# Performance work log

Measured on AMD Instinct MI355X. Metric: run time of the kernel, lower is better.

The kernel has to match this reference:

```python
import jax, jax.numpy as jnp
import numpy as np

QP = 127.0          # signed symmetric 8-bit: Qp = 2**(8-1)-1
MIN_RANGE = 1e-6


def _ste_round(q):
    # round_pass: straight-through estimator round
    return q + jax.lax.stop_gradient(jnp.round(q) - q)


def _quant_per_token(x):
    # symmetric per-token: amax over last dim, keepdim
    s = jnp.clip(jnp.max(jnp.abs(x), axis=-1, keepdims=True), MIN_RANGE, None) / QP
    return _ste_round(x / s), s


def _quant_per_tensor(w):
    s = jnp.clip(jnp.max(jnp.abs(w)), MIN_RANGE, None) / QP
    return _ste_round(w / s), s


def _qlinear(x2d, w, b):
    # fake-quant linear: quantize act per-token, weight per-tensor,
    # int-domain matmul, bias added before dequant rescale (faithful to source)
    qx, sx = _quant_per_token(x2d)      # [N,K], [N,1]
    qw, sw = _quant_per_tensor(w)       # [M,K], scalar
    out = jnp.matmul(qx, qw.T) + b[None, :]
    return out * (sx * sw)              # [N,M]


def setup_inputs() -> dict:
    key = jax.random.key(0)
    k1, k2, k3, k4, k5 = jax.random.split(key, 5)
    B, S, D, H = 64, 197, 768, 3072
    return {
        "x": jax.random.normal(k1, (B, S, D), dtype=jnp.float32),
        "w1": jax.random.normal(k2, (H, D), dtype=jnp.float32) * 0.02,
        "b1": jax.random.normal(k3, (H,), dtype=jnp.float32) * 0.02,
        "w2": jax.random.normal(k4, (D, H), dtype=jnp.float32) * 0.02,
        "b2": jax.random.normal(k5, (D,), dtype=jnp.float32) * 0.02,
    }


def reference(x, w1, b1, w2, b2):
    B, S, D = x.shape
    x2d = x.reshape(-1, D)                         # view(-1, x.size(-1))
    h = _qlinear(x2d, w1, b1)                      # fc1
    h = jax.nn.gelu(h, approximate=False)          # ViT Mlp activation (exact GELU)
    o = _qlinear(h, w2, b2)                        # fc2
    return o.reshape(B, S, -1)
```

## Files before the change

### kernel.cpp

```cpp
#include <hip/hip_runtime.h>
#include <stdint.h>

#define QPF  127.0f
#define MINR 1e-6f

typedef int v4i __attribute__((ext_vector_type(4)));
typedef float f4v __attribute__((ext_vector_type(4)));
typedef _Float16 h4v __attribute__((ext_vector_type(4)));
typedef _Float16 h8 __attribute__((ext_vector_type(8)));
typedef signed char c8 __attribute__((ext_vector_type(8)));

__device__ __forceinline__ float wave_max64(float v) {
  v = fmaxf(v, __shfl_xor(v, 32, 64));
  v = fmaxf(v, __shfl_xor(v, 16, 64));
  v = fmaxf(v, __shfl_xor(v, 8, 64));
  v = fmaxf(v, __shfl_xor(v, 4, 64));
  v = fmaxf(v, __shfl_xor(v, 2, 64));
  v = fmaxf(v, __shfl_xor(v, 1, 64));
  return v;
}

__device__ __forceinline__ float gelu_exact(float x) {
  float z = fabsf(x) * 0.70710678118654752440f;
  float t = __builtin_amdgcn_rcpf(fmaf(0.3275911f, z, 1.0f));
  float p = fmaf(fmaf(fmaf(fmaf(1.061405429f, t, -1.453152027f), t,
                           1.421413741f), t, -0.284496736f), t, 0.254829592f) * t;
  float e = __expf(-z * z);
  float erfz = fmaf(-p, e, 1.0f);
  float cdf = fmaf(0.5f, copysignf(erfz, x), 0.5f);
  return x * cdf;
}

__device__ __forceinline__ void gl2lds16(const void* g, void* l) {
  __builtin_amdgcn_global_load_lds(
      (const __attribute__((address_space(1))) int*)g,
      (__attribute__((address_space(3))) int*)l,
      16, 0, 0);
}

__global__ __launch_bounds__(256) void pre_kernel(
    const float* __restrict__ w1, const float* __restrict__ w2, int n4,
    const float* __restrict__ x, signed char* __restrict__ qx,
    float* __restrict__ sx, unsigned* __restrict__ amaxh,
    float* __restrict__ partial, int K, int nTok) {
  __shared__ float red[4];
  const int b = blockIdx.x;
  const int tid = threadIdx.x;
  const int lane = tid & 63, wvi = tid >> 6;

  if (b < 1024) {
    const float4* w4 = (const float4*)(b < 512 ? w1 : w2);
    const int bb = b & 511;
    float m = 0.f;
    for (int i = bb * 256 + tid; i < n4; i += 512 * 256) {
      float4 v = w4[i];
      m = fmaxf(m, fmaxf(fmaxf(fabsf(v.x), fabsf(v.y)),
                         fmaxf(fabsf(v.z), fabsf(v.w))));
    }
    m = wave_max64(m);
    if (lane == 0) red[wvi] = m;
    __syncthreads();
    if (tid == 0)
      partial[b] = fmaxf(fmaxf(red[0], red[1]), fmaxf(red[2], red[3]));
  } else {
    const int token = b - 1024;
    const float4* xr = (const float4*)(x + (size_t)token * K);
    const int k4 = K >> 2;
    float m = 0.f;
    float4 v = {0.f, 0.f, 0.f, 0.f};
    if (tid < k4) {
      v = xr[tid];
      m = fmaxf(fmaxf(fabsf(v.x), fabsf(v.y)), fmaxf(fabsf(v.z), fabsf(v.w)));
    }
    m = wave_max64(m);
    if (lane == 0) red[wvi] = m;
    __syncthreads();
    const float M = fmaxf(fmaxf(red[0], red[1]), fmaxf(red[2], red[3]));
    const float s = fmaxf(M, MINR) / QPF;
    const float rs = 1.0f / s;
    if (tid == 0) { sx[token] = s; amaxh[token] = 0u; }
    if (tid < k4) {
      char4 c;
      c.x = (signed char)(int)rintf(v.x * rs);
      c.y = (signed char)(int)rintf(v.y * rs);
      c.z = (signed char)(int)rintf(v.z * rs);
      c.w = (signed char)(int)rintf(v.w * rs);
      ((char4*)(qx + (size_t)token * K))[tid] = c;
    }
  }
}

__global__ __launch_bounds__(256) void wquant2_kernel(
    const float* __restrict__ w1, const float* __restrict__ w2, int n4,
    const float* __restrict__ partial, unsigned* __restrict__ wamax,
    signed char* __restrict__ q1, signed char* __restrict__ q2) {
  __shared__ float red[4];
  const int tid = threadIdx.x;
  const int lane = tid & 63, wvi = tid >> 6;
  const int y = blockIdx.y;
  float m = fmaxf(partial[y * 512 + tid], partial[y * 512 + 256 + tid]);
  m = wave_max64(m);
  if (lane == 0) red[wvi] = m;
  __syncthreads();
  const float M = fmaxf(fmaxf(red[0], red[1]), fmaxf(red[2], red[3]));
  if (blockIdx.x == 0 && tid == 0) wamax[y] = __float_as_uint(M);
  const float s = fmaxf(M, MINR) / QPF;
  const float rs = 1.0f / s;
  const float4* w4 = (const float4*)(y ? w2 : w1);
  char4* q4 = (char4*)(y ? q2 : q1);
  for (int i = blockIdx.x * 256 + tid; i < n4; i += gridDim.x * 256) {
    float4 v = w4[i];
    char4 c;
    c.x = (signed char)(int)rintf(v.x * rs);
    c.y = (signed char)(int)rintf(v.y * rs);
    c.z = (signed char)(int)rintf(v.z * rs);
    c.w = (signed char)(int)rintf(v.w * rs);
    q4[i] = c;
  }
}

__global__ __launch_bounds__(256) void hquant4_kernel(
    const _Float16* __restrict__ h, const unsigned* __restrict__ amaxbits,
    signed char* __restrict__ qh, float* __restrict__ sh, int K) {
  const int token = blockIdx.x * 4 + (threadIdx.x >> 6);
  const int lane = threadIdx.x & 63;
  const float s = fmaxf(__uint_as_float(amaxbits[token]), MINR) / QPF;
  const float rs = 1.0f / s;
  if (lane == 0) sh[token] = s;
  const h8* hr = (const h8*)(h + (size_t)token * K);
  c8* qr = (c8*)(qh + (size_t)token * K);
  for (int i = lane; i < (K >> 3); i += 64) {
    h8 v = hr[i];
    c8 c;
#pragma unroll
    for (int j = 0; j < 8; j++)
      c[j] = (signed char)(int)rintf((float)v[j] * rs);
    qr[i] = c;
  }
}

__global__ __launch_bounds__(256, 2) void gemm1_i8(
    const signed char* __restrict__ A, const signed char* __restrict__ B,
    const float* __restrict__ bias, const float* __restrict__ sA,
    const unsigned* __restrict__ sBbits, _Float16* __restrict__ out,
    unsigned* __restrict__ amax_out, int N, int K, int Mout) {
  __shared__ __align__(16) signed char lds[3 * 16384];

  const int t = threadIdx.x;
  const int lane = t & 63;
  const int wv = t >> 6;
  const int wm = wv >> 1;
  const int wn = wv & 1;
  const int rowBlk = blockIdx.y * 128;
  const int colBlk = blockIdx.x * 128;

  int ar0 = rowBlk + wv * 16 + (lane >> 2);
  int ar1 = ar0 + 64;
  if (ar0 > N - 1) ar0 = N - 1;
  if (ar1 > N - 1) ar1 = N - 1;
  const int br0 = colBlk + wv * 16 + (lane >> 2);
  const int br1 = br0 + 64;
  const int kb = (((lane & 3) ^ ((lane >> 3) & 3)) * 16);

  const signed char* gA0 = A + (size_t)ar0 * K + kb;
  const signed char* gA1 = A + (size_t)ar1 * K + kb;
  const signed char* gB0 = B + (size_t)br0 * K + kb;
  const signed char* gB1 = B + (size_t)br1 * K + kb;

  const v4i vzero = {0, 0, 0, 0};
  v4i acc[4][4];
#pragma unroll
  for (int i = 0; i < 4; i++)
#pragma unroll
    for (int j = 0; j < 4; j++) acc[i][j] = vzero;

  const int swz = ((lane >> 4) ^ ((lane >> 1) & 3)) * 16;
  const int aoff = (wm * 64 + (lane & 15)) * 64 + swz;
  const int boff = (wn * 64 + (lane & 15)) * 64 + swz + 8192;

  const int T = K >> 6;

  auto issue = [&](int bufo) {
    signed char* a = lds + bufo + wv * 1024;
    gl2lds16(gA0, a);
    gl2lds16(gA1, a + 4096);
    gl2lds16(gB0, a + 8192);
    gl2lds16(gB1, a + 12288);
    gA0 += 64; gA1 += 64; gB0 += 64; gB1 += 64;
  };

  issue(0);
  issue(16384);

  int cur = 0;
  for (int kt = 0; kt < T; ++kt) {
    asm volatile("" ::: "memory");
    if (kt < T - 1)
      __builtin_amdgcn_s_waitcnt(0x0074);
    else
      __builtin_amdgcn_s_waitcnt(0x0070);
    __builtin_amdgcn_s_barrier();
    asm volatile("" ::: "memory");

    if (kt + 2 < T) {
      int pf = cur + 32768;
      if (pf >= 49152) pf -= 49152;
      issue(pf);
    }

    v4i a[4], b[4];
#pragma unroll
    for (int mi = 0; mi < 4; mi++)
      a[mi] = *(const v4i*)(lds + cur + aoff + mi * 1024);
#pragma unroll
    for (int ni = 0; ni < 4; ni++)
      b[ni] = *(const v4i*)(lds + cur + boff + ni * 1024);
#pragma unroll
    for (int mi = 0; mi < 4; mi++)
#pragma unroll
      for (int ni = 0; ni < 4; ni++)
        acc[mi][ni] = __builtin_amdgcn_mfma_i32_16x16x64_i8(b[ni], a[mi],
                                                            acc[mi][ni], 0, 0, 0);
    cur += 16384;
    if (cur >= 49152) cur = 0;
  }

  const float sB = fmaxf(__uint_as_float(*sBbits), MINR) / QPF;
  const int col0 = colBlk + wn * 64 + (lane >> 4) * 4;

  f4v bv[4];
#pragma unroll
  for (int ni = 0; ni < 4; ni++) bv[ni] = *(const f4v*)(bias + col0 + ni * 16);

#pragma unroll
  for (int mi = 0; mi < 4; mi++) {
    const int grow = rowBlk + wm * 64 + mi * 16 + (lane & 15);
    const float ss = ((grow < N) ? sA[grow] : 0.f) * sB;
    float rmax = 0.f;
#pragma unroll
    for (int ni = 0; ni < 4; ni++) {
      h4v hv;
#pragma unroll
      for (int r = 0; r < 4; r++) {
        float v = ((float)acc[mi][ni][r] + bv[ni][r]) * ss;
        v = gelu_exact(v);
        rmax = fmaxf(rmax, fabsf(v));
        hv[r] = (_Float16)v;
      }
      if (grow < N)
        *(h4v*)(out + (size_t)grow * Mout + col0 + ni * 16) = hv;
    }
    rmax = fmaxf(rmax, __shfl_xor(rmax, 16, 64));
    rmax = fmaxf(rmax, __shfl_xor(rmax, 32, 64));
    if (lane < 16 && grow < N)
      atomicMax(amax_out + grow, __float_as_uint(rmax));
  }
}

__global__ __launch_bounds__(128, 2) void gemm2_i8(
    const signed char* __restrict__ A, const signed char* __restrict__ B,
    const float* __restrict__ bias, const float* __restrict__ sA,
    const unsigned* __restrict__ sBbits, float* __restrict__ out,
    int N, int K, int Mout) {
  __shared__ __align__(16) signed char lds[3 * 12288];

  const int t = threadIdx.x;
  const int lane = t & 63;
  const int wv = t >> 6;
  const int rowBlk = blockIdx.y * 128;
  const int colBlk = blockIdx.x * 64;

  const int trow = t >> 2;
  const int kb = (((t & 3) ^ ((t >> 3) & 3)) * 16);

  int ar[4];
#pragma unroll
  for (int i = 0; i < 4; i++) {
    ar[i] = rowBlk + i * 32 + trow;
    if (ar[i] > N - 1) ar[i] = N - 1;
  }
  const signed char* gA0 = A + (size_t)ar[0] * K + kb;
  const signed char* gA1 = A + (size_t)ar[1] * K + kb;
  const signed char* gA2 = A + (size_t)ar[2] * K + kb;
  const signed char* gA3 = A + (size_t)ar[3] * K + kb;
  const signed char* gB0 = B + (size_t)(colBlk + trow) * K + kb;
  const signed char* gB1 = B + (size_t)(colBlk + 32 + trow) * K + kb;

  const v4i vzero = {0, 0, 0, 0};
  v4i acc[4][4];
#pragma unroll
  for (int i = 0; i < 4; i++)
#pragma unroll
    for (int j = 0; j < 4; j++) acc[i][j] = vzero;

  const int swz = ((lane >> 4) ^ ((lane >> 1) & 3)) * 16;
  const int aoff = (wv * 64 + (lane & 15)) * 64 + swz;
  const int boff = 8192 + (lane & 15) * 64 + swz;

  const int T = K >> 6;

  auto issue = [&](int bufo) {
    signed char* p = lds + bufo + t * 16;
    gl2lds16(gA0, p);
    gl2lds16(gA1, p + 2048);
    gl2lds16(gA2, p + 4096);
    gl2lds16(gA3, p + 6144);
    gl2lds16(gB0, p + 8192);
    gl2lds16(gB1, p + 10240);
    gA0 += 64; gA1 += 64; gA2 += 64; gA3 += 64; gB0 += 64; gB1 += 64;
  };

  issue(0);
  issue(12288);

  int cur = 0;
  for (int kt = 0; kt < T; ++kt) {
    asm volatile("" ::: "memory");
    if (kt < T - 1)
      __builtin_amdgcn_s_waitcnt(0x0076);
    else
      __builtin_amdgcn_s_waitcnt(0x0070);
    __builtin_amdgcn_s_barrier();
    asm volatile("" ::: "memory");

    if (kt + 2 < T) {
      int pf = cur + 24576;
      if (pf >= 36864) pf -= 36864;
      issue(pf);
    }

    v4i a[4], b[4];
#pragma unroll
    for (int mi = 0; mi < 4; mi++)
      a[mi] = *(const v4i*)(lds + cur + aoff + mi * 1024);
#pragma unroll
    for (int ni = 0; ni < 4; ni++)
      b[ni] = *(const v4i*)(lds + cur + boff + ni * 1024);
#pragma unroll
    for (int mi = 0; mi < 4; mi++)
#pragma unroll
      for (int ni = 0; ni < 4; ni++)
        acc[mi][ni] = __builtin_amdgcn_mfma_i32_16x16x64_i8(b[ni], a[mi],
                                                            acc[mi][ni], 0, 0, 0);
    cur += 12288;
    if (cur >= 36864) cur = 0;
  }

  const float sB = fmaxf(__uint_as_float(*sBbits), MINR) / QPF;
  const int col0 = colBlk + (lane >> 4) * 4;

  f4v bv[4];
#pragma unroll
  for (int ni = 0; ni < 4; ni++) bv[ni] = *(const f4v*)(bias + col0 + ni * 16);

#pragma unroll
  for (int mi = 0; mi < 4; mi++) {
    const int grow = rowBlk + wv * 64 + mi * 16 + (lane & 15);
    const float ss = ((grow < N) ? sA[grow] : 0.f) * sB;
#pragma unroll
    for (int ni = 0; ni < 4; ni++) {
      f4v o;
#pragma unroll
      for (int r = 0; r < 4; r++)
        o[r] = ((float)acc[mi][ni][r] + bv[ni][r]) * ss;
      if (grow < N)
        *(f4v*)(out + (size_t)grow * Mout + col0 + ni * 16) = o;
    }
  }
}

extern "C" void kernel_launch(void* const* d_in, const int* in_sizes, int n_in,
                              void* d_out, int out_size, void* d_ws, size_t ws_size,
                              hipStream_t stream) {
  const float* x  = (const float*)d_in[0];
  const float* w1 = (const float*)d_in[1];
  const float* b1 = (const float*)d_in[2];
  const float* w2 = (const float*)d_in[3];
  const float* b2 = (const float*)d_in[4];

  const int H = in_sizes[2];
  const int D = in_sizes[4];
  const int N = in_sizes[0] / D;
  float* out = (float*)d_out;

  char* ws = (char*)d_ws;
  auto alloc = [&](size_t bytes) {
    char* p = ws;
    ws += (bytes + 255) & ~(size_t)255;
    return p;
  };
  signed char* qx  = (signed char*)alloc((size_t)N * D);
  signed char* qw1 = (signed char*)alloc((size_t)H * D);
  signed char* qw2 = (signed char*)alloc((size_t)H * D);
  signed char* qh  = (signed char*)alloc((size_t)N * H);
  float*    sx     = (float*)alloc((size_t)N * 4);
  float*    sh     = (float*)alloc((size_t)N * 4);
  unsigned* amaxh  = (unsigned*)alloc((size_t)N * 4);
  unsigned* wamax  = (unsigned*)alloc(256);
  float*    partial= (float*)alloc(1024 * 4);
  _Float16* h      = (_Float16*)alloc((size_t)N * H * 2);
  (void)ws_size;

  const int n4w = (H * D) >> 2;

  pre_kernel<<<1024 + N, 256, 0, stream>>>(w1, w2, n4w, x, qx, sx, amaxh,
                                           partial, D, N);
  wquant2_kernel<<<dim3(512, 2), 256, 0, stream>>>(w1, w2, n4w, partial, wamax,
                                                   qw1, qw2);

  dim3 g1(H / 128, (N + 127) / 128);
  gemm1_i8<<<g1, 256, 0, stream>>>(qx, qw1, b1, sx, wamax + 0, h, amaxh,
                                   N, D, H);
  hquant4_kernel<<<N / 4, 256, 0, stream>>>(h, amaxh, qh, sh, H);

  dim3 g2(D / 64, (N + 127) / 128);
  gemm2_i8<<<g2, 128, 0, stream>>>(qh, qw2, b2, sh, wamax + 1, out, N, H, D);
}
```

Measured before the change: 255.4 us.

## Widen gemm2 tiles to 128x128, add XCD swizzle, batch per-token quant per wave

```diff
diff --git a/kernel.cpp b/kernel.cpp
--- a/kernel.cpp
+++ b/kernel.cpp
@@ -38,6 +38,14 @@
       16, 0, 0);
 }
 
+__device__ __forceinline__ int xcd_swizzle(int flat, int nwg) {
+  const int xcd = flat & 7;
+  const int idx = flat >> 3;
+  const int q = nwg >> 3, r = nwg & 7;
+  const int base = (xcd < r) ? xcd * (q + 1) : r * (q + 1) + (xcd - r) * q;
+  return base + idx;
+}
+
 __global__ __launch_bounds__(256) void pre_kernel(
     const float* __restrict__ w1, const float* __restrict__ w2, int n4,
     const float* __restrict__ x, signed char* __restrict__ qx,
@@ -63,29 +71,30 @@
     if (tid == 0)
       partial[b] = fmaxf(fmaxf(red[0], red[1]), fmaxf(red[2], red[3]));
   } else {
-    const int token = b - 1024;
-    const float4* xr = (const float4*)(x + (size_t)token * K);
-    const int k4 = K >> 2;
-    float m = 0.f;
-    float4 v = {0.f, 0.f, 0.f, 0.f};
-    if (tid < k4) {
-      v = xr[tid];
-      m = fmaxf(fmaxf(fabsf(v.x), fabsf(v.y)), fmaxf(fabsf(v.z), fabsf(v.w)));
-    }
-    m = wave_max64(m);
-    if (lane == 0) red[wvi] = m;
-    __syncthreads();
-    const float M = fmaxf(fmaxf(red[0], red[1]), fmaxf(red[2], red[3]));
-    const float s = fmaxf(M, MINR) / QPF;
-    const float rs = 1.0f / s;
-    if (tid == 0) { sx[token] = s; amaxh[token] = 0u; }
-    if (tid < k4) {
-      char4 c;
-      c.x = (signed char)(int)rintf(v.x * rs);
-      c.y = (signed char)(int)rintf(v.y * rs);
-      c.z = (signed char)(int)rintf(v.z * rs);
-      c.w = (signed char)(int)rintf(v.w * rs);
-      ((char4*)(qx + (size_t)token * K))[tid] = c;
+    const int token = (b - 1024) * 4 + wvi;
+    if (token < nTok) {
+      const int k4 = K >> 2;
+      const float4* xr = (const float4*)(x + (size_t)token * K);
+      float m = 0.f;
+      for (int i = lane; i < k4; i += 64) {
+        float4 v = xr[i];
+        m = fmaxf(m, fmaxf(fmaxf(fabsf(v.x), fabsf(v.y)),
+                           fmaxf(fabsf(v.z), fabsf(v.w))));
+      }
+      m = wave_max64(m);
+      const float s = fmaxf(m, MINR) / QPF;
+      const float rs = 1.0f / s;
+      if (lane == 0) { sx[token] = s; amaxh[token] = 0u; }
+      char4* q4 = (char4*)(qx + (size_t)token * K);
+      for (int i = lane; i < k4; i += 64) {
+        float4 v = xr[i];
+        char4 c;
+        c.x = (signed char)(int)rintf(v.x * rs);
+        c.y = (signed char)(int)rintf(v.y * rs);
+        c.z = (signed char)(int)rintf(v.z * rs);
+        c.w = (signed char)(int)rintf(v.w * rs);
+        q4[i] = c;
+      }
     }
   }
 }
@@ -151,8 +160,11 @@
   const int wv = t >> 6;
   const int wm = wv >> 1;
   const int wn = wv & 1;
-  const int rowBlk = blockIdx.y * 128;
-  const int colBlk = blockIdx.x * 128;
+
+  const int nwg = gridDim.x * gridDim.y;
+  const int wg = xcd_swizzle(blockIdx.x + gridDim.x * blockIdx.y, nwg);
+  const int colBlk = (wg % gridDim.x) * 128;
+  const int rowBlk = (wg / gridDim.x) * 128;
 
   int ar0 = rowBlk + wv * 16 + (lane >> 2);
   int ar1 = ar0 + 64;
@@ -257,34 +269,36 @@
   }
 }
 
-__global__ __launch_bounds__(128, 2) void gemm2_i8(
+__global__ __launch_bounds__(256, 2) void gemm2_i8(
     const signed char* __restrict__ A, const signed char* __restrict__ B,
     const float* __restrict__ bias, const float* __restrict__ sA,
     const unsigned* __restrict__ sBbits, float* __restrict__ out,
     int N, int K, int Mout) {
-  __shared__ __align__(16) signed char lds[3 * 12288];
+  __shared__ __align__(16) signed char lds[3 * 16384];
 
   const int t = threadIdx.x;
   const int lane = t & 63;
   const int wv = t >> 6;
-  const int rowBlk = blockIdx.y * 128;
-  const int colBlk = blockIdx.x * 64;
-
-  const int trow = t >> 2;
-  const int kb = (((t & 3) ^ ((t >> 3) & 3)) * 16);
-
-  int ar[4];
-#pragma unroll
-  for (int i = 0; i < 4; i++) {
-    ar[i] = rowBlk + i * 32 + trow;
-    if (ar[i] > N - 1) ar[i] = N - 1;
-  }
-  const signed char* gA0 = A + (size_t)ar[0] * K + kb;
-  const signed char* gA1 = A + (size_t)ar[1] * K + kb;
-  const signed char* gA2 = A + (size_t)ar[2] * K + kb;
-  const signed char* gA3 = A + (size_t)ar[3] * K + kb;
-  const signed char* gB0 = B + (size_t)(colBlk + trow) * K + kb;
-  const signed char* gB1 = B + (size_t)(colBlk + 32 + trow) * K + kb;
+  const int wm = wv >> 1;
+  const int wn = wv & 1;
+
+  const int nwg = gridDim.x * gridDim.y;
+  const int wg = xcd_swizzle(blockIdx.x + gridDim.x * blockIdx.y, nwg);
+  const int colBlk = (wg % gridDim.x) * 128;
+  const int rowBlk = (wg / gridDim.x) * 128;
+
+  int ar0 = rowBlk + wv * 16 + (lane >> 2);
+  int ar1 = ar0 + 64;
+  if (ar0 > N - 1) ar0 = N - 1;
+  if (ar1 > N - 1) ar1 = N - 1;
+  const int br0 = colBlk + wv * 16 + (lane >> 2);
+  const int br1 = br0 + 64;
+  const int kb = (((lane & 3) ^ ((lane >> 3) & 3)) * 16);
+
+  const signed char* gA0 = A + (size_t)ar0 * K + kb;
+  const signed char* gA1 = A + (size_t)ar1 * K + kb;
+  const signed char* gB0 = B + (size_t)br0 * K + kb;
+  const signed char* gB1 = B + (size_t)br1 * K + kb;
 
   const v4i vzero = {0, 0, 0, 0};
   v4i acc[4][4];
@@ -294,38 +308,36 @@
     for (int j = 0; j < 4; j++) acc[i][j] = vzero;
 
   const int swz = ((lane >> 4) ^ ((lane >> 1) & 3)) * 16;
-  const int aoff = (wv * 64 + (lane & 15)) * 64 + swz;
-  const int boff = 8192 + (lane & 15) * 64 + swz;
+  const int aoff = (wm * 64 + (lane & 15)) * 64 + swz;
+  const int boff = (wn * 64 + (lane & 15)) * 64 + swz + 8192;
 
   const int T = K >> 6;
 
   auto issue = [&](int bufo) {
-    signed char* p = lds + bufo + t * 16;
-    gl2lds16(gA0, p);
-    gl2lds16(gA1, p + 2048);
-    gl2lds16(gA2, p + 4096);
-    gl2lds16(gA3, p + 6144);
-    gl2lds16(gB0, p + 8192);
-    gl2lds16(gB1, p + 10240);
-    gA0 += 64; gA1 += 64; gA2 += 64; gA3 += 64; gB0 += 64; gB1 += 64;
+    signed char* a = lds + bufo + wv * 1024;
+    gl2lds16(gA0, a);
+    gl2lds16(gA1, a + 4096);
+    gl2lds16(gB0, a + 8192);
+    gl2lds16(gB1, a + 12288);
+    gA0 += 64; gA1 += 64; gB0 += 64; gB1 += 64;
   };
 
   issue(0);
-  issue(12288);
+  issue(16384);
 
   int cur = 0;
   for (int kt = 0; kt < T; ++kt) {
     asm volatile("" ::: "memory");
     if (kt < T - 1)
-      __builtin_amdgcn_s_waitcnt(0x0076);
+      __builtin_amdgcn_s_waitcnt(0x0074);
     else
       __builtin_amdgcn_s_waitcnt(0x0070);
     __builtin_amdgcn_s_barrier();
     asm volatile("" ::: "memory");
 
     if (kt + 2 < T) {
-      int pf = cur + 24576;
-      if (pf >= 36864) pf -= 36864;
+      int pf = cur + 32768;
+      if (pf >= 49152) pf -= 49152;
       issue(pf);
     }
 
@@ -342,12 +354,12 @@
       for (int ni = 0; ni < 4; ni++)
         acc[mi][ni] = __builtin_amdgcn_mfma_i32_16x16x64_i8(b[ni], a[mi],
                                                             acc[mi][ni], 0, 0, 0);
-    cur += 12288;
-    if (cur >= 36864) cur = 0;
+    cur += 16384;
+    if (cur >= 49152) cur = 0;
   }
 
   const float sB = fmaxf(__uint_as_float(*sBbits), MINR) / QPF;
-  const int col0 = colBlk + (lane >> 4) * 4;
+  const int col0 = colBlk + wn * 64 + (lane >> 4) * 4;
 
   f4v bv[4];
 #pragma unroll
@@ -355,7 +367,7 @@
 
 #pragma unroll
   for (int mi = 0; mi < 4; mi++) {
-    const int grow = rowBlk + wv * 64 + mi * 16 + (lane & 15);
+    const int grow = rowBlk + wm * 64 + mi * 16 + (lane & 15);
     const float ss = ((grow < N) ? sA[grow] : 0.f) * sB;
 #pragma unroll
     for (int ni = 0; ni < 4; ni++) {
@@ -403,8 +415,8 @@
 
   const int n4w = (H * D) >> 2;
 
-  pre_kernel<<<1024 + N, 256, 0, stream>>>(w1, w2, n4w, x, qx, sx, amaxh,
-                                           partial, D, N);
+  pre_kernel<<<1024 + (N + 3) / 4, 256, 0, stream>>>(w1, w2, n4w, x, qx, sx,
+                                                     amaxh, partial, D, N);
   wquant2_kernel<<<dim3(512, 2), 256, 0, stream>>>(w1, w2, n4w, partial, wamax,
                                                    qw1, qw2);
 
@@ -413,6 +425,6 @@
                                    N, D, H);
   hquant4_kernel<<<N / 4, 256, 0, stream>>>(h, amaxh, qh, sh, H);
 
-  dim3 g2(D / 64, (N + 127) / 128);
-  gemm2_i8<<<g2, 128, 0, stream>>>(qh, qw2, b2, sh, wamax + 1, out, N, H, D);
-}
+  dim3 g2(D / 128, (N + 127) / 128);
+  gemm2_i8<<<g2, 256, 0, stream>>>(qh, qw2, b2, sh, wamax + 1, out, N, H, D);
+}
```

Measured after the change: 234.3 us, median of 2. 8.3% less time.
